# Optimization experiments

Measured on AMD Instinct MI355X. Metric: run time of the kernel, lower is better.

Reference implementation:

```python
import jax, jax.numpy as jnp
import numpy as np

ALPHA = 0.2  # LeakyReLU negative slope
NEG_INF = -9e15

def setup_inputs() -> dict:
    key = jax.random.key(0)
    k1, k2, k3, k4, k5 = jax.random.split(key, 5)
    B, N, Fin, Fout = 8, 2048, 128, 128
    h = jax.random.normal(k1, (B, N, Fin), dtype=jnp.float32)
    adj = jax.random.randint(k2, (N, N), 0, 2, dtype=jnp.int32)
    dist = jax.random.uniform(k3, (N, N), dtype=jnp.float32)
    W = jax.random.normal(k4, (Fin, Fout), dtype=jnp.float32) * (1.414 * (6.0 / (Fin + Fout)) ** 0.5)
    a = jax.random.normal(k5, (2 * Fout, 1), dtype=jnp.float32) * 0.1
    distance_scaler = jnp.ones((1,), dtype=jnp.float32)
    return {"h": h, "adj": adj, "dist": dist, "W": W, "a": a, "distance_scaler": distance_scaler}

def reference(h, adj, dist, W, a, distance_scaler):
    # h: [B,N,Fin], adj/dist: [N,N], W: [Fin,Fout], a: [2*Fout,1]
    h_prime = jnp.einsum('bnf,fh->bnh', h, W)              # [B,N,Fout]
    Fout = h_prime.shape[-1]
    a1, a2 = a[:Fout, 0], a[Fout:, 0]
    # additive score: a1.h_i + a2.h_j, equivalent to cat([h_i,h_j]) @ a
    si = h_prime @ a1                                      # [B,N]
    sj = h_prime @ a2                                      # [B,N]
    e = jax.nn.leaky_relu(si[:, :, None] + sj[:, None, :], negative_slope=ALPHA)  # [B,N,N]
    dist_bias = -jnp.log(dist + 1e-6) * distance_scaler[0]  # [N,N]
    scores = e + dist_bias[None, :, :]
    scores = jnp.where(adj[None, :, :] > 0, scores, NEG_INF)
    attention = jax.nn.softmax(scores, axis=2)             # [B,N,N]
    # dropout=identity in eval mode
    out = jnp.einsum('bij,bjh->bih', attention, h_prime)   # [B,N,Fout]
    return jax.nn.elu(out)
```

## Files before the change

### kernel.cpp

```cpp
#include <hip/hip_runtime.h>
#include <hip/hip_bf16.h>

typedef __attribute__((ext_vector_type(4))) float f32x4;
typedef __attribute__((ext_vector_type(8))) short short8;
typedef __attribute__((ext_vector_type(4))) unsigned short ushort4v;
typedef _Float16 f16x8 __attribute__((ext_vector_type(8)));

#define NB 8
#define NN 2048
#define NF 128
#define LOG2E 1.4426950408889634f
#define MASK_NEG_H -60000.0f

static __device__ __forceinline__ unsigned short f2bf(float f) {
    union { __hip_bfloat16 b; unsigned short u; } cv;
    cv.b = __float2bfloat16(f);
    return cv.u;
}

static __device__ __forceinline__ void gload_lds16(const void* g, void* l) {
    __builtin_amdgcn_global_load_lds(
        (const __attribute__((address_space(1))) unsigned int*)g,
        (__attribute__((address_space(3))) unsigned int*)l, 16, 0, 0);
}

__global__ __launch_bounds__(256) void k_pre(
    const float* __restrict__ h, const int* __restrict__ adj,
    const float* __restrict__ dist, const float* __restrict__ W,
    const float* __restrict__ a, const float* __restrict__ scaler,
    unsigned short* __restrict__ vfrag, float* __restrict__ siC,
    float* __restrict__ sjC, _Float16* __restrict__ biasF)
{
    __shared__ __align__(16) unsigned char smem[34816];
    const int bid = blockIdx.x;
    const int t = threadIdx.x;

    if (bid < 256) {
        unsigned char* WT = smem;
        float* wa1 = (float*)(smem + 32768);
        float* wa2 = wa1 + NF;

        const int lane = t & 63;
        const int w = t >> 6;
        const int b = bid >> 5;
        const int i0 = (bid & 31) << 6;

        {
            const int f = t >> 1;
            const int c0 = (t & 1) << 6;
            float s1 = 0.f, s2 = 0.f;
            const float* wrow = W + f * NF + c0;
            const float* a1p = a + c0;
            const float* a2p = a + NF + c0;
            #pragma unroll 8
            for (int c = 0; c < 64; ++c) {
                float wv = wrow[c];
                s1 += wv * a1p[c];
                s2 += wv * a2p[c];
                int col = c0 + c;
                int dst = col * 256 + ((2 * f) ^ ((col & 15) << 4));
                *reinterpret_cast<unsigned short*>(&WT[dst]) = f2bf(wv);
            }
            s1 += __shfl_xor(s1, 1);
            s2 += __shfl_xor(s2, 1);
            if ((t & 1) == 0) { wa1[f] = s1 * LOG2E; wa2[f] = s2 * LOG2E; }
        }
        __syncthreads();

        const int l15 = lane & 15;
        const int arow = i0 + w * 16 + l15;
        const int kofs = (lane >> 4) << 3;
        const float* hrow = h + (size_t)(b * NN + arow) * NF + kofs;
        const int swz = l15 << 4;

        f32x4 acc[8];
        #pragma unroll
        for (int nt = 0; nt < 8; ++nt) acc[nt] = (f32x4)(0.f);
        float s1 = 0.f, s2 = 0.f;

        #pragma unroll
        for (int k0 = 0; k0 < NF; k0 += 32) {
            f32x4 h0 = *reinterpret_cast<const f32x4*>(hrow + k0);
            f32x4 h1 = *reinterpret_cast<const f32x4*>(hrow + k0 + 4);
            f32x4 w1lo = *reinterpret_cast<const f32x4*>(&wa1[k0 + kofs]);
            f32x4 w1hi = *reinterpret_cast<const f32x4*>(&wa1[k0 + kofs + 4]);
            f32x4 w2lo = *reinterpret_cast<const f32x4*>(&wa2[k0 + kofs]);
            f32x4 w2hi = *reinterpret_cast<const f32x4*>(&wa2[k0 + kofs + 4]);
            short8 af;
            #pragma unroll
            for (int e = 0; e < 4; ++e) {
                s1 += h0[e] * w1lo[e] + h1[e] * w1hi[e];
                s2 += h0[e] * w2lo[e] + h1[e] * w2hi[e];
                af[e]     = (short)f2bf(h0[e]);
                af[4 + e] = (short)f2bf(h1[e]);
            }
            const int ib = (2 * (k0 + kofs)) ^ swz;
            #pragma unroll
            for (int nt = 0; nt < 8; ++nt) {
                short8 bf8 = *reinterpret_cast<short8*>(&WT[(nt * 16 + l15) * 256 + ib]);
                acc[nt] = __builtin_amdgcn_mfma_f32_16x16x32_bf16(af, bf8, acc[nt], 0, 0, 0);
            }
        }

        s1 += __shfl_xor(s1, 16); s1 += __shfl_xor(s1, 32);
        s2 += __shfl_xor(s2, 16); s2 += __shfl_xor(s2, 32);
        if (lane < 16) {
            siC[b * NN + arow] = s1;
            sjC[b * NN + arow] = s2;
        }

        const int J0 = i0 + w * 16 + ((lane >> 4) << 2);
        const int s = J0 >> 5;
        const int jq = (J0 >> 3) & 3;
        const int eh = J0 & 7;
        #pragma unroll
        for (int nt = 0; nt < 8; ++nt) {
            ushort4v pk;
            #pragma unroll
            for (int e = 0; e < 4; ++e) pk[e] = f2bf(acc[nt][e]);
            *reinterpret_cast<ushort4v*>(
                vfrag + (((size_t)(b * 64 + s) * 8 + nt) * 64 + (l15 | (jq << 4))) * 8 + eh) = pk;
        }
    } else {
        _Float16 (*st)[64][8] = (_Float16 (*)[64][8])smem;
        const int bid2 = bid - 256;
        const int iblk = bid2 >> 3;
        const int jch = bid2 & 7;
        const int i_l = t >> 4;
        const int o2 = t & 15;
        const int i = iblk * 16 + i_l;
        const int jbase = jch * 256 + o2 * 16;
        const float sc = scaler[0];

        const int* ap = adj + (size_t)i * NN + jbase;
        const float* dp = dist + (size_t)i * NN + jbase;
        int av[16]; float dv[16];
        *reinterpret_cast<int4*>(&av[0])  = *reinterpret_cast<const int4*>(ap);
        *reinterpret_cast<int4*>(&av[4])  = *reinterpret_cast<const int4*>(ap + 4);
        *reinterpret_cast<int4*>(&av[8])  = *reinterpret_cast<const int4*>(ap + 8);
        *reinterpret_cast<int4*>(&av[12]) = *reinterpret_cast<const int4*>(ap + 12);
        *reinterpret_cast<float4*>(&dv[0])  = *reinterpret_cast<const float4*>(dp);
        *reinterpret_cast<float4*>(&dv[4])  = *reinterpret_cast<const float4*>(dp + 4);
        *reinterpret_cast<float4*>(&dv[8])  = *reinterpret_cast<const float4*>(dp + 8);
        *reinterpret_cast<float4*>(&dv[12]) = *reinterpret_cast<const float4*>(dp + 12);

        #pragma unroll
        for (int u = 0; u < 2; ++u) {
            const int sl = (o2 * 2 + u) >> 2;
            const int jq = (o2 * 2 + u) & 3;
            f16x8 pk;
            #pragma unroll
            for (int e = 0; e < 8; ++e) {
                const int idx = u * 8 + e;
                float v = (av[idx] > 0) ? (-__log2f(dv[idx] + 1e-6f) * sc) : MASK_NEG_H;
                pk[e] = (_Float16)v;
            }
            *reinterpret_cast<f16x8*>(&st[sl][i_l | (jq << 4)][0]) = pk;
        }
        __syncthreads();

        const int w = t >> 6, lane = t & 63;
        #pragma unroll
        for (int sub = 0; sub < 2; ++sub) {
            const int fs = w * 2 + sub;
            *reinterpret_cast<f16x8*>(
                biasF + ((size_t)(iblk * 64 + jch * 8 + fs) * 64 + lane) * 8) =
                *reinterpret_cast<f16x8*>(&st[fs][lane][0]);
        }
    }
}

__global__ __launch_bounds__(512) void k_attn(
    const unsigned short* __restrict__ vfrag, const float* __restrict__ siC,
    const float* __restrict__ sjC, const _Float16* __restrict__ biasF,
    float* __restrict__ out)
{
    __shared__ __align__(16) unsigned char vbuf[4][24576];
    __shared__ float lp[2][4][16];

    const int t = threadIdx.x;
    const int lane = t & 63;
    const int w = t >> 6;
    const int rt = w & 3;
    const int jh = w >> 2;
    const int l15 = lane & 15;
    const int hi = lane >> 4;

    const int b = blockIdx.x & 7;
    const int rg = blockIdx.x >> 3;

    const int rowbase = rg * 64 + rt * 16;
    const float si0 = siC[b * NN + rowbase + l15];

    const float* sjb = sjC + b * NN + hi * 8;
    const unsigned short* vsrcb = vfrag + (size_t)b * 262144 + w * 512 + lane * 8;
    const _Float16* bsrcb = biasF + ((size_t)((rg * 4 + (w & 3)) * 64) * 64 + lane) * 8;

    f32x4 acc[8];
    #pragma unroll
    for (int ct = 0; ct < 8; ++ct) acc[ct] = (f32x4)(0.f);
    float ls0 = 0.f;
    f32x4 sjA0, sjA1;

#define STAGE(TL)                                                             \
    { unsigned char* lb = &vbuf[(TL) & 3][w * 1024];                          \
      const unsigned short* gsV = vsrcb + (TL) * 8192;                        \
      gload_lds16(gsV,        lb);                                            \
      gload_lds16(gsV + 4096, lb + 8192);                                     \
      gload_lds16(bsrcb + (size_t)(2 * (TL) + (w >> 2)) * 512,                \
                  &vbuf[(TL) & 3][16384 + w * 1024]); }

#define PF_SJ(TL)                                                             \
    { const int sA = 2 * (TL) + jh;                                           \
      sjA0 = *reinterpret_cast<const f32x4*>(sjb + sA * 32);                  \
      sjA1 = *reinterpret_cast<const f32x4*>(sjb + sA * 32 + 4); }

#define QSTEP(BUF)                                                            \
    { const f16x8 bv = *reinterpret_cast<const f16x8*>(                       \
          &vbuf[BUF][16384 + (jh * 4 + rt) * 1024 + lane * 16]);              \
      short8 pa;                                                              \
      _Pragma("unroll")                                                       \
      for (int e = 0; e < 8; ++e) {                                           \
          const float sjv = (e < 4) ? sjA0[e] : sjA1[e - 4];                  \
          float x = si0 + sjv;                                                \
          x = fmaxf(x, 0.2f * x) + (float)bv[e];                              \
          float p = __builtin_amdgcn_exp2f(x);                                \
          ls0 += p;                                                           \
          pa[e] = (short)f2bf(p);                                             \
      }                                                                       \
      __builtin_amdgcn_s_setprio(1);                                          \
      _Pragma("unroll")                                                       \
      for (int ct = 0; ct < 8; ++ct) {                                        \
          const short8 bfr = *reinterpret_cast<const short8*>(                \
              &vbuf[BUF][jh * 8192 + ct * 1024 + lane * 16]);                 \
          acc[ct] = __builtin_amdgcn_mfma_f32_16x16x32_bf16(pa, bfr, acc[ct], 0, 0, 0); \
      }                                                                       \
      __builtin_amdgcn_s_setprio(0); }

    STAGE(0)
    PF_SJ(0)
    asm volatile("" ::: "memory");
    STAGE(1)
    STAGE(2)

    for (int tl = 0; tl < 30; ++tl) {
        asm volatile("s_waitcnt vmcnt(3)" ::: "memory");
        __builtin_amdgcn_s_barrier();
        QSTEP(tl & 3)
        PF_SJ(tl + 1)
        asm volatile("" ::: "memory");
        if (tl < 29) STAGE(tl + 3)
    }
    asm volatile("s_waitcnt vmcnt(3)" ::: "memory");
    __builtin_amdgcn_s_barrier();
    QSTEP(2)
    PF_SJ(31)
    asm volatile("s_waitcnt vmcnt(0)" ::: "memory");
    __builtin_amdgcn_s_barrier();
    QSTEP(3)

#undef STAGE
#undef PF_SJ
#undef QSTEP

    ls0 += __shfl_xor(ls0, 16);
    ls0 += __shfl_xor(ls0, 32);
    if (lane < 16) lp[jh][rt][l15] = ls0;
    __syncthreads();

    if (jh == 1) {
        #pragma unroll
        for (int ct = 0; ct < 8; ++ct)
            *reinterpret_cast<f32x4*>(
                &vbuf[0][((rt * 8 + ct) * 64 + lane) * 16 % 24576 +
                         (((rt * 8 + ct) * 64 + lane) * 16 / 24576) * 24576]) = acc[ct];
    }
    __syncthreads();
    if (jh == 0) {
        float linv[4];
        #pragma unroll
        for (int e = 0; e < 4; ++e) {
            const int rr = (hi << 2) + e;
            linv[e] = 1.0f / (lp[0][rt][rr] + lp[1][rt][rr]);
        }
        #pragma unroll
        for (int ct = 0; ct < 8; ++ct) {
            const int off = ((rt * 8 + ct) * 64 + lane) * 16;
            f32x4 o = acc[ct] + *reinterpret_cast<const f32x4*>(
                &vbuf[0][off % 24576 + (off / 24576) * 24576]);
            const int col = ct * 16 + l15;
            #pragma unroll
            for (int e = 0; e < 4; ++e) {
                const int row = rowbase + (hi << 2) + e;
                float v = o[e] * linv[e];
                v = (v > 0.f) ? v : expm1f(v);
                out[(size_t)(b * NN + row) * NF + col] = v;
            }
        }
    }
}

extern "C" void kernel_launch(void* const* d_in, const int* in_sizes, int n_in,
                              void* d_out, int out_size, void* d_ws, size_t ws_size,
                              hipStream_t stream) {
    (void)in_sizes; (void)n_in; (void)out_size; (void)ws_size;
    const float* h      = (const float*)d_in[0];
    const int*   adj    = (const int*)d_in[1];
    const float* dist   = (const float*)d_in[2];
    const float* W      = (const float*)d_in[3];
    const float* a      = (const float*)d_in[4];
    const float* scaler = (const float*)d_in[5];
    float* out = (float*)d_out;

    char* ws = (char*)d_ws;
    unsigned short* vfrag = (unsigned short*)ws;
    float* siC      = (float*)(ws + 4 * 1024 * 1024);
    float* sjC      = (float*)(ws + 4 * 1024 * 1024 + 65536);
    _Float16* biasF = (_Float16*)(ws + 4 * 1024 * 1024 + 2 * 65536);

    k_pre<<<dim3(1280), dim3(256), 0, stream>>>(h, adj, dist, W, a, scaler,
                                                vfrag, siC, sjC, biasF);
    k_attn<<<dim3(NB * NN / 64), dim3(512), 0, stream>>>(vfrag, siC, sjC, biasF, out);
}
```

Measured before the change: 49.52 us.

## Split attention blocks into 32-row tiles with column-half waves and register-loaded bias

The attention kernel now handles 32 query rows per block instead of 64, which doubles the grid. Waves are split by row tile, key half and output-column half, so each wave issues 4 MFMAs per step instead of 8. The bias tile and sj values are now loaded straight into registers rather than staged through LDS. The LDS ring shrinks to 3 buffers of 16KB, and the pipeline depth and wait counts are adjusted to match. The aim is better CU occupancy and load balance. The cost is that the exp/softmax work is duplicated across the two column-half waves and V is read from global memory twice as often.

```diff
diff --git a/kernel.cpp b/kernel.cpp
--- a/kernel.cpp
+++ b/kernel.cpp
@@ -175,53 +175,52 @@
     const float* __restrict__ sjC, const _Float16* __restrict__ biasF,
     float* __restrict__ out)
 {
-    __shared__ __align__(16) unsigned char vbuf[4][24576];
-    __shared__ float lp[2][4][16];
+    __shared__ __align__(16) unsigned char vbuf[3][16384];
+    __shared__ float lp[2][2][16];
 
     const int t = threadIdx.x;
     const int lane = t & 63;
     const int w = t >> 6;
-    const int rt = w & 3;
-    const int jh = w >> 2;
+    const int rt = w & 1;
+    const int jh = (w >> 1) & 1;
+    const int ch = w >> 2;
     const int l15 = lane & 15;
     const int hi = lane >> 4;
 
     const int b = blockIdx.x & 7;
     const int rg = blockIdx.x >> 3;
 
-    const int rowbase = rg * 64 + rt * 16;
+    const int rowbase = rg * 32 + rt * 16;
     const float si0 = siC[b * NN + rowbase + l15];
 
     const float* sjb = sjC + b * NN + hi * 8;
-    const unsigned short* vsrcb = vfrag + (size_t)b * 262144 + w * 512 + lane * 8;
-    const _Float16* bsrcb = biasF + ((size_t)((rg * 4 + (w & 3)) * 64) * 64 + lane) * 8;
-
-    f32x4 acc[8];
+    const unsigned short* vsrcb = vfrag + (size_t)b * 262144 + t * 8;
+    const _Float16* bp = biasF + ((size_t)((rg * 2 + rt) * 64) * 64 + lane) * 8;
+
+    f32x4 acc[4];
     #pragma unroll
-    for (int ct = 0; ct < 8; ++ct) acc[ct] = (f32x4)(0.f);
+    for (int k = 0; k < 4; ++k) acc[k] = (f32x4)(0.f);
     float ls0 = 0.f;
-    f32x4 sjA0, sjA1;
+    f32x4 sj0, sj1;
+    f16x8 bv;
 
 #define STAGE(TL)                                                             \
-    { unsigned char* lb = &vbuf[(TL) & 3][w * 1024];                          \
-      const unsigned short* gsV = vsrcb + (TL) * 8192;                        \
-      gload_lds16(gsV,        lb);                                            \
-      gload_lds16(gsV + 4096, lb + 8192);                                     \
-      gload_lds16(bsrcb + (size_t)(2 * (TL) + (w >> 2)) * 512,                \
-                  &vbuf[(TL) & 3][16384 + w * 1024]); }
-
-#define PF_SJ(TL)                                                             \
-    { const int sA = 2 * (TL) + jh;                                           \
-      sjA0 = *reinterpret_cast<const f32x4*>(sjb + sA * 32);                  \
-      sjA1 = *reinterpret_cast<const f32x4*>(sjb + sA * 32 + 4); }
+    { unsigned char* lb = &vbuf[(TL) % 3][t * 16];                            \
+      const unsigned short* gs = vsrcb + (TL) * 8192;                         \
+      gload_lds16(gs,        lb);                                             \
+      gload_lds16(gs + 4096, lb + 8192); }
+
+#define PF_SB(TL)                                                             \
+    { const int s = 2 * (TL) + jh;                                            \
+      sj0 = *reinterpret_cast<const f32x4*>(sjb + s * 32);                    \
+      sj1 = *reinterpret_cast<const f32x4*>(sjb + s * 32 + 4);                \
+      bv  = *reinterpret_cast<const f16x8*>(bp + s * 512); }
 
 #define QSTEP(BUF)                                                            \
-    { const f16x8 bv = *reinterpret_cast<const f16x8*>(                       \
-          &vbuf[BUF][16384 + (jh * 4 + rt) * 1024 + lane * 16]);              \
-      short8 pa;                                                              \
+    { short8 pa;                                                              \
       _Pragma("unroll")                                                       \
       for (int e = 0; e < 8; ++e) {                                           \
-          const float sjv = (e < 4) ? sjA0[e] : sjA1[e - 4];                  \
+          const float sjv = (e < 4) ? sj0[e] : sj1[e - 4];                    \
           float x = si0 + sjv;                                                \
           x = fmaxf(x, 0.2f * x) + (float)bv[e];                              \
           float p = __builtin_amdgcn_exp2f(x);                                \
@@ -230,53 +229,47 @@
       }                                                                       \
       __builtin_amdgcn_s_setprio(1);                                          \
       _Pragma("unroll")                                                       \
-      for (int ct = 0; ct < 8; ++ct) {                                        \
+      for (int k = 0; k < 4; ++k) {                                           \
           const short8 bfr = *reinterpret_cast<const short8*>(                \
-              &vbuf[BUF][jh * 8192 + ct * 1024 + lane * 16]);                 \
-          acc[ct] = __builtin_amdgcn_mfma_f32_16x16x32_bf16(pa, bfr, acc[ct], 0, 0, 0); \
+              &vbuf[BUF][jh * 8192 + (ch * 4 + k) * 1024 + lane * 16]);       \
+          acc[k] = __builtin_amdgcn_mfma_f32_16x16x32_bf16(pa, bfr, acc[k], 0, 0, 0); \
       }                                                                       \
       __builtin_amdgcn_s_setprio(0); }
 
     STAGE(0)
-    PF_SJ(0)
+    PF_SB(0)
     asm volatile("" ::: "memory");
     STAGE(1)
-    STAGE(2)
-
-    for (int tl = 0; tl < 30; ++tl) {
-        asm volatile("s_waitcnt vmcnt(3)" ::: "memory");
+
+    for (int tl = 0; tl < 31; ++tl) {
+        asm volatile("s_waitcnt vmcnt(5)" ::: "memory");
         __builtin_amdgcn_s_barrier();
-        QSTEP(tl & 3)
-        PF_SJ(tl + 1)
+        QSTEP(tl % 3)
+        PF_SB(tl + 1)
         asm volatile("" ::: "memory");
-        if (tl < 29) STAGE(tl + 3)
+        if (tl + 2 < 32) STAGE(tl + 2)
     }
     asm volatile("s_waitcnt vmcnt(3)" ::: "memory");
     __builtin_amdgcn_s_barrier();
-    QSTEP(2)
-    PF_SJ(31)
-    asm volatile("s_waitcnt vmcnt(0)" ::: "memory");
-    __builtin_amdgcn_s_barrier();
-    QSTEP(3)
+    QSTEP(31 % 3)
 
 #undef STAGE
-#undef PF_SJ
+#undef PF_SB
 #undef QSTEP
 
     ls0 += __shfl_xor(ls0, 16);
     ls0 += __shfl_xor(ls0, 32);
-    if (lane < 16) lp[jh][rt][l15] = ls0;
-    __syncthreads();
+    if (ch == 0 && lane < 16) lp[jh][rt][l15] = ls0;
 
     if (jh == 1) {
-        #pragma unroll
-        for (int ct = 0; ct < 8; ++ct)
-            *reinterpret_cast<f32x4*>(
-                &vbuf[0][((rt * 8 + ct) * 64 + lane) * 16 % 24576 +
-                         (((rt * 8 + ct) * 64 + lane) * 16 / 24576) * 24576]) = acc[ct];
+        float* red = (float*)&vbuf[0][(rt * 2 + ch) * 4096];
+        #pragma unroll
+        for (int k = 0; k < 4; ++k)
+            *reinterpret_cast<f32x4*>(&red[(k * 64 + lane) * 4]) = acc[k];
     }
     __syncthreads();
     if (jh == 0) {
+        const float* red = (const float*)&vbuf[0][(rt * 2 + ch) * 4096];
         float linv[4];
         #pragma unroll
         for (int e = 0; e < 4; ++e) {
@@ -284,11 +277,9 @@
             linv[e] = 1.0f / (lp[0][rt][rr] + lp[1][rt][rr]);
         }
         #pragma unroll
-        for (int ct = 0; ct < 8; ++ct) {
-            const int off = ((rt * 8 + ct) * 64 + lane) * 16;
-            f32x4 o = acc[ct] + *reinterpret_cast<const f32x4*>(
-                &vbuf[0][off % 24576 + (off / 24576) * 24576]);
-            const int col = ct * 16 + l15;
+        for (int k = 0; k < 4; ++k) {
+            f32x4 o = acc[k] + *reinterpret_cast<const f32x4*>(&red[(k * 64 + lane) * 4]);
+            const int col = ch * 64 + k * 16 + l15;
             #pragma unroll
             for (int e = 0; e < 4; ++e) {
                 const int row = rowbase + (hi << 2) + e;
@@ -320,5 +311,5 @@
 
     k_pre<<<dim3(1280), dim3(256), 0, stream>>>(h, adj, dist, W, a, scaler,
                                                 vfrag, siC, sjC, biasF);
-    k_attn<<<dim3(NB * NN / 64), dim3(512), 0, stream>>>(vfrag, siC, sjC, biasF, out);
-}
+    k_attn<<<dim3(NB * NN / 32), dim3(512), 0, stream>>>(vfrag, siC, sjC, biasF, out);
+}
```

After: 51.90 us. 1.05x slower.
